# Kernel optimization log

Measured on AMD Instinct MI355X. Metric: run time of the kernel, lower is better.

## Reference

```python
import jax, jax.numpy as jnp
import numpy as np

B, C, CE, DK, DV, H, W = 2, 64, 96, 64, 64, 96, 96
EPS = 1e-6


def setup_inputs() -> dict:
    key = jax.random.key(0)
    ks = jax.random.split(key, 8)
    s = lambda fan_in: 1.0 / np.sqrt(fan_in)
    return {
        "x": jax.random.normal(ks[0], (B, C, H, W), jnp.float32),
        "x_enc": jax.random.normal(ks[1], (B, CE, H, W), jnp.float32),
        "Wq": jax.random.uniform(ks[2], (DK, CE), jnp.float32, -s(CE), s(CE)),
        "bq": jax.random.uniform(ks[3], (DK,), jnp.float32, -s(CE), s(CE)),
        "Wk": jax.random.uniform(ks[4], (DK, CE), jnp.float32, -s(CE), s(CE)),
        "bk": jax.random.uniform(ks[5], (DK,), jnp.float32, -s(CE), s(CE)),
        "Wv": jax.random.uniform(ks[6], (DV, C), jnp.float32, -s(C), s(C)),
        "bv": jax.random.uniform(ks[7], (DV,), jnp.float32, -s(C), s(C)),
    }


def _l2norm(t):
    # F.normalize(dim=1): divide by channel-dim L2 norm, clamped at eps
    n = jnp.maximum(jnp.linalg.norm(t, axis=1, keepdims=True), EPS)
    return t / n


def reference(x, x_enc, Wq, bq, Wk, bk, Wv, bv):
    # 1x1 conv projections == pointwise channel GEMMs
    Q = jnp.einsum('oc,bchw->bohw', Wq, x_enc) + bq[None, :, None, None]
    K = jnp.einsum('oc,bchw->bohw', Wk, x_enc) + bk[None, :, None, None]
    V = jnp.einsum('oc,bchw->bohw', Wv, x) + bv[None, :, None, None]
    vshape = V.shape
    Q = _l2norm(Q.reshape(B, DK, H * W))  # [B, dk, L]
    K = _l2norm(K.reshape(B, DK, H * W))
    V = V.reshape(B, DV, H * W)           # [B, dv, L]
    # cosine-similarity attention over all spatial positions: A is [B, L, L]
    A = jax.nn.softmax(jnp.einsum('bqi,bqj->bij', Q, K), axis=-1)
    R = jnp.einsum('bij,bvj->bvi', A, V)   # [B, dv, L]
    return R.reshape(vshape)
```

## Files before the change

kernel.cpp:

```cpp
#include <hip/hip_runtime.h>

#define L_ 9216

typedef unsigned int uint;
typedef unsigned short ushort;
typedef __attribute__((ext_vector_type(8))) short short8;
typedef __attribute__((ext_vector_type(4))) float f32x4;
typedef __attribute__((ext_vector_type(16))) float f32x16;
typedef __attribute__((ext_vector_type(4))) unsigned uint4v;
typedef __attribute__((ext_vector_type(2))) unsigned uint2v;

#define MFMA32(a, b, c) __builtin_amdgcn_mfma_f32_32x32x16_bf16(a, b, c, 0, 0, 0)

#if __has_builtin(__builtin_amdgcn_exp2f)
#define EXP2(x) __builtin_amdgcn_exp2f(x)
#else
#define EXP2(x) exp2f(x)
#endif

#define GLOAD_LDS16(g, l)                                            \
  __builtin_amdgcn_global_load_lds(                                  \
      (const __attribute__((address_space(1))) unsigned int*)(g),    \
      (__attribute__((address_space(3))) unsigned int*)(l), 16, 0, 0)

union B8 {
  uint4v u;
  short8 s;
};

__device__ __forceinline__ ushort f2bf(float f) {
  uint u = __float_as_uint(f);
  return (ushort)((u + 0x7fffu + ((u >> 16) & 1u)) >> 16);
}

__device__ __forceinline__ f32x16 zero16() {
  f32x16 v;
#pragma unroll
  for (int i = 0; i < 16; i++) v[i] = 0.f;
  return v;
}

__global__ __launch_bounds__(256) void prep_kernel(
    const float* __restrict__ Wq, const float* __restrict__ Wk,
    const float* __restrict__ Wv, ushort* __restrict__ Wqb,
    ushort* __restrict__ Wkb, ushort* __restrict__ Wvb) {
  int i = blockIdx.x * 256 + threadIdx.x;
  if (i < 6144) {
    Wqb[i] = f2bf(Wq[i]);
    Wkb[i] = f2bf(Wk[i]);
  }
  if (i < 4096) Wvb[i] = f2bf(Wv[i]);
}

template <int CC, int TASK>
__device__ __forceinline__ void projm_body(
    const float* __restrict__ X,
    const ushort* __restrict__ Wb,
    const float* __restrict__ bias,
    ushort* __restrict__ dst) {
  constexpr int NKT = CC / 16;
  const int bx = blockIdx.x;
  const int b = bx / 288;
  const int p0 = (bx - b * 288) * 32;
  const int lane = threadIdx.x;
  const int ql = lane & 31;
  const int hs = lane >> 5;

  const float* Xb = X + (size_t)b * CC * L_ + p0 + ql;
  float xv[NKT * 8];
#pragma unroll
  for (int kt = 0; kt < NKT; kt++)
#pragma unroll
    for (int i = 0; i < 8; i++)
      xv[kt * 8 + i] = Xb[(size_t)(kt * 16 + hs * 8 + i) * L_];

  B8 bfr[NKT];
#pragma unroll
  for (int kt = 0; kt < NKT; kt++)
#pragma unroll
    for (int j = 0; j < 4; j++) {
      uint lo = f2bf(xv[kt * 8 + 2 * j]);
      uint hi = f2bf(xv[kt * 8 + 2 * j + 1]);
      bfr[kt].u[j] = lo | (hi << 16);
    }

  const ushort* Wr0 = Wb + (size_t)ql * CC + hs * 8;
  const ushort* Wr1 = Wb + (size_t)(32 + ql) * CC + hs * 8;

  f32x16 a0 = zero16(), a1 = zero16();
#pragma unroll
  for (int kt = 0; kt < NKT; kt++) {
    short8 w0 = *(const short8*)(Wr0 + kt * 16);
    short8 w1 = *(const short8*)(Wr1 + kt * 16);
    a0 = MFMA32(w0, bfr[kt].s, a0);
    a1 = MFMA32(w1, bfr[kt].s, a1);
  }

#pragma unroll
  for (int g = 0; g < 4; g++) {
    float4 b0 = *(const float4*)(bias + 8 * g + 4 * hs);
    float4 b1 = *(const float4*)(bias + 32 + 8 * g + 4 * hs);
    a0[4 * g + 0] += b0.x; a0[4 * g + 1] += b0.y;
    a0[4 * g + 2] += b0.z; a0[4 * g + 3] += b0.w;
    a1[4 * g + 0] += b1.x; a1[4 * g + 1] += b1.y;
    a1[4 * g + 2] += b1.z; a1[4 * g + 3] += b1.w;
  }

  if (TASK < 2) {
    float ss = 0.f;
#pragma unroll
    for (int r = 0; r < 16; r++) ss += a0[r] * a0[r] + a1[r] * a1[r];
    ss += __shfl_xor(ss, 32);
    float i0 = 1.0f / fmaxf(sqrtf(ss), 1e-6f);
    if (TASK == 0) i0 *= 1.44269504f;
    uint* d = (uint*)(dst + ((size_t)(b * L_ + p0 + ql)) * 64);
#pragma unroll
    for (int g = 0; g < 4; g++) {
      uint2v u0, u1;
      u0[0] = (uint)f2bf(a0[4 * g + 0] * i0) | ((uint)f2bf(a0[4 * g + 1] * i0) << 16);
      u0[1] = (uint)f2bf(a0[4 * g + 2] * i0) | ((uint)f2bf(a0[4 * g + 3] * i0) << 16);
      u1[0] = (uint)f2bf(a1[4 * g + 0] * i0) | ((uint)f2bf(a1[4 * g + 1] * i0) << 16);
      u1[1] = (uint)f2bf(a1[4 * g + 2] * i0) | ((uint)f2bf(a1[4 * g + 3] * i0) << 16);
      *(uint2v*)(d + 4 * g + 2 * hs) = u0;
      *(uint2v*)(d + 16 + 4 * g + 2 * hs) = u1;
    }
  } else {
#pragma unroll
    for (int r = 0; r < 16; r++) {
      int dv0 = (r & 3) + 8 * (r >> 2) + 4 * hs;
      dst[(size_t)(b * 64 + dv0) * L_ + p0 + ql] = f2bf(a0[r]);
      dst[(size_t)(b * 64 + 32 + dv0) * L_ + p0 + ql] = f2bf(a1[r]);
    }
  }
}

__global__ __launch_bounds__(64) void projm_kernel(
    const float* __restrict__ x, const float* __restrict__ x_enc,
    const ushort* __restrict__ Wqb, const float* __restrict__ bq,
    const ushort* __restrict__ Wkb, const float* __restrict__ bk,
    const ushort* __restrict__ Wvb, const float* __restrict__ bv,
    ushort* __restrict__ Qb, ushort* __restrict__ Kb,
    ushort* __restrict__ Vb) {
  const int task = blockIdx.y;
  if (task == 0)
    projm_body<96, 0>(x_enc, Wqb, bq, Qb);
  else if (task == 1)
    projm_body<96, 1>(x_enc, Wkb, bk, Kb);
  else
    projm_body<64, 2>(x, Wvb, bv, Vb);
}

__global__ __launch_bounds__(512, 4) void attn_kernel(
    const ushort* __restrict__ Qb, const ushort* __restrict__ Kb,
    const ushort* __restrict__ Vb, ushort* __restrict__ OP,
    float* __restrict__ LB, int tps) {
  __shared__ __align__(16) ushort K_l[3][64 * 64];
  __shared__ __align__(16) ushort V_l[3][64 * 64];

  const int nwg = gridDim.x;
  const int chunk = nwg >> 3;
  const int bid = blockIdx.x;
  const int logical = (bid & 7) * chunk + (bid >> 3);
  const int split = logical / 72;
  const int qidx = logical - split * 72;
  const int b = qidx / 36;
  const int q0 = (qidx - b * 36) * 256;

  const int t = threadIdx.x;
  const int lane = t & 63;
  const int w = t >> 6;
  const int ql = lane & 31;
  const int hs = lane >> 5;

  const ushort* Kg = Kb + (size_t)b * L_ * 64;
  const ushort* Vg = Vb + (size_t)b * 64 * L_;

  const int qrow = q0 + w * 32 + ql;
  const ushort* Qr = Qb + ((size_t)(b * L_ + qrow)) * 64 + hs * 8;
  short8 qf[4];
  qf[0] = *(const short8*)(Qr);
  qf[1] = *(const short8*)(Qr + 16);
  qf[2] = *(const short8*)(Qr + 32);
  qf[3] = *(const short8*)(Qr + 48);

  B8 onesu;
  onesu.u[0] = 0x3F803F80u;
  onesu.u[1] = 0x3F803F80u;
  onesu.u[2] = 0x3F803F80u;
  onesu.u[3] = 0x3F803F80u;

  f32x16 o[2];
  o[0] = zero16();
  o[1] = zero16();
  f32x16 od = zero16();

  const int rr = t >> 3, pl = t & 7;
  const int psrc = (pl ^ (rr & 7)) << 3;
  const int j0base = split * tps * 64;

#define STAGE(buf, j0)                                                       \
  {                                                                          \
    GLOAD_LDS16(Kg + (size_t)(j0)*64 + rr * 64 + psrc, &K_l[buf][w * 512]);  \
    GLOAD_LDS16(Vg + (size_t)rr * L_ + (j0) + psrc, &V_l[buf][w * 512]);     \
  }

  STAGE(0, j0base);
  STAGE(1, j0base + 64);

  int cur = 0;
  for (int tt = 0; tt < tps; tt++) {
    if (tt + 1 < tps) {
      asm volatile("s_waitcnt vmcnt(2)" ::: "memory");
    } else {
      asm volatile("s_waitcnt vmcnt(0)" ::: "memory");
    }
    __builtin_amdgcn_s_barrier();
    __builtin_amdgcn_sched_barrier(0);
    if (tt + 2 < tps) {
      int nb = cur + 2;
      if (nb >= 3) nb -= 3;
      STAGE(nb, j0base + (tt + 2) * 64);
    }
    const ushort* Kc = K_l[cur];
    const ushort* Vc = V_l[cur];

    B8 pf[4];
#pragma unroll
    for (int st = 0; st < 2; st++) {
      const int krow = st * 32 + ql;
      const int ksw = (krow & 7) << 3;
      f32x16 sa = zero16();
      __builtin_amdgcn_s_setprio(1);
#pragma unroll
      for (int m = 0; m < 4; m++) {
        short8 kf = *(const short8*)&Kc[(krow * 64 + m * 16 + hs * 8) ^ ksw];
        sa = MFMA32(kf, qf[m], sa);
      }
      __builtin_amdgcn_s_setprio(0);
      uint Wp[8];
#pragma unroll
      for (int c = 0; c < 4; c++)
#pragma unroll
        for (int rp = 0; rp < 2; rp++) {
          int i0 = 4 * c + 2 * rp;
          float p0 = EXP2(sa[i0]);
          float p1 = EXP2(sa[i0 + 1]);
          Wp[2 * c + rp] = __builtin_amdgcn_perm(
              __float_as_uint(p1), __float_as_uint(p0), 0x07060302u);
        }
#pragma unroll
      for (int u = 0; u < 2; u++) {
        auto ra = __builtin_amdgcn_permlane32_swap(Wp[4 * u + 0], Wp[4 * u + 2],
                                                   false, false);
        auto rb = __builtin_amdgcn_permlane32_swap(Wp[4 * u + 1], Wp[4 * u + 3],
                                                   false, false);
        uint4v fw;
        fw[0] = ra[0];
        fw[1] = rb[0];
        fw[2] = ra[1];
        fw[3] = rb[1];
        pf[st * 2 + u].u = fw;
      }
    }

    __builtin_amdgcn_s_setprio(1);
#pragma unroll
    for (int s = 0; s < 4; s++) od = MFMA32(onesu.s, pf[s].s, od);

#pragma unroll
    for (int dt = 0; dt < 2; dt++) {
      const int vrow = dt * 32 + ql;
      const int vsw = (vrow & 7) << 3;
#pragma unroll
      for (int s = 0; s < 4; s++) {
        short8 vf = *(const short8*)&Vc[(vrow * 64 + s * 16 + hs * 8) ^ vsw];
        o[dt] = MFMA32(vf, pf[s].s, o[dt]);
      }
    }
    __builtin_amdgcn_s_setprio(0);

    cur = (cur + 1 == 3) ? 0 : cur + 1;
  }

  if (hs == 0) LB[(size_t)split * 2 * L_ + (size_t)b * L_ + qrow] = od[0];

  ushort* Ob = OP + (size_t)split * 2 * 64 * L_;
#pragma unroll
  for (int dt = 0; dt < 2; dt++)
#pragma unroll
    for (int r = 0; r < 16; r++) {
      int dv = dt * 32 + (r & 3) + 8 * (r >> 2) + 4 * hs;
      Ob[(size_t)(b * 64 + dv) * L_ + qrow] = f2bf(o[dt][r]);
    }
}

template <int NS>
__global__ __launch_bounds__(256) void combine_kernel(
    const ushort* __restrict__ OP, const float* __restrict__ LB,
    float* __restrict__ out) {
  const size_t e = ((size_t)blockIdx.x * 256 + threadIdx.x) * 8;
  const int bdv = (int)(e / L_);
  const int b = bdv >> 6;
  const int q = (int)(e % L_);
  float os[8], ls[8];
#pragma unroll
  for (int i = 0; i < 8; i++) { os[i] = 0.f; ls[i] = 0.f; }
#pragma unroll
  for (int s = 0; s < NS; s++) {
    uint4v pv = *(const uint4v*)(OP + (size_t)s * 2 * 64 * L_ + e);
    const float* lp = LB + (size_t)s * 2 * L_ + (size_t)b * L_ + q;
    f32x4 l0 = *(const f32x4*)(lp);
    f32x4 l1 = *(const f32x4*)(lp + 4);
#pragma unroll
    for (int i = 0; i < 4; i++) {
      os[2 * i] += __uint_as_float(pv[i] << 16);
      os[2 * i + 1] += __uint_as_float(pv[i] & 0xFFFF0000u);
      ls[i] += l0[i];
      ls[4 + i] += l1[i];
    }
  }
  float r[8];
#pragma unroll
  for (int i = 0; i < 8; i++) r[i] = os[i] / ls[i];
  *(f32x4*)(out + e) = *(const f32x4*)&r[0];
  *(f32x4*)(out + e + 4) = *(const f32x4*)&r[4];
}

extern "C" void kernel_launch(void* const* d_in, const int* in_sizes, int n_in,
                              void* d_out, int out_size, void* d_ws, size_t ws_size,
                              hipStream_t stream) {
  const float* x = (const float*)d_in[0];
  const float* x_enc = (const float*)d_in[1];
  const float* Wq = (const float*)d_in[2];
  const float* bq = (const float*)d_in[3];
  const float* Wk = (const float*)d_in[4];
  const float* bk = (const float*)d_in[5];
  const float* Wv = (const float*)d_in[6];
  const float* bv = (const float*)d_in[7];
  float* out = (float*)d_out;

  ushort* Qb = (ushort*)d_ws;
  ushort* Kb = Qb + (size_t)2 * L_ * 64;
  ushort* Vb = Kb + (size_t)2 * L_ * 64;
  ushort* Wqb = Vb + (size_t)2 * L_ * 64;
  ushort* Wkb = Wqb + 6144;
  ushort* Wvb = Wkb + 6144;
  const size_t qkv_bytes = (size_t)3 * 2 * L_ * 64 * 2 + 2 * (6144 + 6144 + 4096);
  const size_t per_split = (size_t)2 * 64 * L_ * 2 + (size_t)2 * L_ * 4;

  int SPLIT = 16;
  while (SPLIT > 1 && qkv_bytes + (size_t)SPLIT * per_split > ws_size) SPLIT >>= 1;

  ushort* OP = (ushort*)((char*)d_ws + qkv_bytes);
  float* LB = (float*)(OP + (size_t)SPLIT * 2 * 64 * L_);

  prep_kernel<<<24, 256, 0, stream>>>(Wq, Wk, Wv, Wqb, Wkb, Wvb);
  projm_kernel<<<dim3(576, 3), 64, 0, stream>>>(x, x_enc, Wqb, bq, Wkb, bk,
                                                Wvb, bv, Qb, Kb, Vb);
  attn_kernel<<<72 * SPLIT, 512, 0, stream>>>(Qb, Kb, Vb, OP, LB, 144 / SPLIT);
  const int cgrid = (2 * 64 * L_ / 8) / 256;
  if (SPLIT == 16)
    combine_kernel<16><<<cgrid, 256, 0, stream>>>(OP, LB, out);
  else if (SPLIT == 8)
    combine_kernel<8><<<cgrid, 256, 0, stream>>>(OP, LB, out);
  else if (SPLIT == 4)
    combine_kernel<4><<<cgrid, 256, 0, stream>>>(OP, LB, out);
  else if (SPLIT == 2)
    combine_kernel<2><<<cgrid, 256, 0, stream>>>(OP, LB, out);
  else
    combine_kernel<1><<<cgrid, 256, 0, stream>>>(OP, LB, out);
}
```

Baseline: 84.83 us.

## Give each attention wave two query tiles, halve block size, double-buffer K/V

Each wave now handles 64 query rows as two 32-row tiles and reuses every K and V fragment it reads from LDS for both tiles, which halves LDS reads per MFMA. The block shrinks to 256 threads, staging moves from a triple buffer to a double buffer with a plain __syncthreads, and each thread issues twice as many loads per stage. The row-sum is now accumulated in scalar registers and reduced with a lane shuffle, replacing the MFMA against a ones matrix. Register pressure roughly doubles and occupancy may fall, and the shallower pipeline may expose more load latency.

Result: slower. 89.57 us (+5.6%).

```diff
diff --git a/kernel.cpp b/kernel.cpp
--- a/kernel.cpp
+++ b/kernel.cpp
@@ -150,12 +150,12 @@
     projm_body<64, 2>(x, Wvb, bv, Vb);
 }
 
-__global__ __launch_bounds__(512, 4) void attn_kernel(
+__global__ __launch_bounds__(256) void attn_kernel(
     const ushort* __restrict__ Qb, const ushort* __restrict__ Kb,
     const ushort* __restrict__ Vb, ushort* __restrict__ OP,
     float* __restrict__ LB, int tps) {
-  __shared__ __align__(16) ushort K_l[3][64 * 64];
-  __shared__ __align__(16) ushort V_l[3][64 * 64];
+  __shared__ __align__(16) ushort K_l[2][4096];
+  __shared__ __align__(16) ushort V_l[2][4096];
 
   const int nwg = gridDim.x;
   const int chunk = nwg >> 3;
@@ -175,98 +175,92 @@
   const ushort* Kg = Kb + (size_t)b * L_ * 64;
   const ushort* Vg = Vb + (size_t)b * 64 * L_;
 
-  const int qrow = q0 + w * 32 + ql;
-  const ushort* Qr = Qb + ((size_t)(b * L_ + qrow)) * 64 + hs * 8;
-  short8 qf[4];
-  qf[0] = *(const short8*)(Qr);
-  qf[1] = *(const short8*)(Qr + 16);
-  qf[2] = *(const short8*)(Qr + 32);
-  qf[3] = *(const short8*)(Qr + 48);
-
-  B8 onesu;
-  onesu.u[0] = 0x3F803F80u;
-  onesu.u[1] = 0x3F803F80u;
-  onesu.u[2] = 0x3F803F80u;
-  onesu.u[3] = 0x3F803F80u;
-
-  f32x16 o[2];
-  o[0] = zero16();
-  o[1] = zero16();
-  f32x16 od = zero16();
+  const int qrowA = q0 + w * 64 + ql;
+  const int qrowB = qrowA + 32;
+  const ushort* QrA = Qb + ((size_t)(b * L_ + qrowA)) * 64 + hs * 8;
+  const ushort* QrB = Qb + ((size_t)(b * L_ + qrowB)) * 64 + hs * 8;
+  short8 qfA[4], qfB[4];
+#pragma unroll
+  for (int m = 0; m < 4; m++) {
+    qfA[m] = *(const short8*)(QrA + m * 16);
+    qfB[m] = *(const short8*)(QrB + m * 16);
+  }
+
+  f32x16 oA[2], oB[2];
+  oA[0] = zero16(); oA[1] = zero16();
+  oB[0] = zero16(); oB[1] = zero16();
+  float psA = 0.f, psB = 0.f;
 
   const int rr = t >> 3, pl = t & 7;
   const int psrc = (pl ^ (rr & 7)) << 3;
   const int j0base = split * tps * 64;
 
-#define STAGE(buf, j0)                                                       \
-  {                                                                          \
-    GLOAD_LDS16(Kg + (size_t)(j0)*64 + rr * 64 + psrc, &K_l[buf][w * 512]);  \
-    GLOAD_LDS16(Vg + (size_t)rr * L_ + (j0) + psrc, &V_l[buf][w * 512]);     \
+#define STAGE(buf, j0)                                                      \
+  {                                                                         \
+    GLOAD_LDS16(Kg + (size_t)(j0)*64 + rr * 64 + psrc, &K_l[buf][w * 512]); \
+    GLOAD_LDS16(Kg + (size_t)(j0)*64 + (rr + 32) * 64 + psrc,               \
+                &K_l[buf][2048 + w * 512]);                                 \
+    GLOAD_LDS16(Vg + (size_t)rr * L_ + (j0) + psrc, &V_l[buf][w * 512]);    \
+    GLOAD_LDS16(Vg + (size_t)(rr + 32) * L_ + (j0) + psrc,                  \
+                &V_l[buf][2048 + w * 512]);                                 \
+  }
+
+#define SMPACK(sa, ps, pf, st)                                              \
+  {                                                                         \
+    uint Wp[8];                                                             \
+    _Pragma("unroll") for (int c = 0; c < 4; c++) _Pragma("unroll")         \
+        for (int rp = 0; rp < 2; rp++) {                                    \
+      int i0 = 4 * c + 2 * rp;                                              \
+      float p0 = EXP2(sa[i0]);                                              \
+      float p1 = EXP2(sa[i0 + 1]);                                          \
+      ps += p0 + p1;                                                        \
+      Wp[2 * c + rp] = __builtin_amdgcn_perm(__float_as_uint(p1),           \
+                                             __float_as_uint(p0),           \
+                                             0x07060302u);                  \
+    }                                                                       \
+    _Pragma("unroll") for (int u = 0; u < 2; u++) {                         \
+      auto ra = __builtin_amdgcn_permlane32_swap(Wp[4 * u + 0],             \
+                                                 Wp[4 * u + 2], false,      \
+                                                 false);                    \
+      auto rb = __builtin_amdgcn_permlane32_swap(Wp[4 * u + 1],             \
+                                                 Wp[4 * u + 3], false,      \
+                                                 false);                    \
+      uint4v fw;                                                            \
+      fw[0] = ra[0];                                                        \
+      fw[1] = rb[0];                                                        \
+      fw[2] = ra[1];                                                        \
+      fw[3] = rb[1];                                                        \
+      pf[(st)*2 + u].u = fw;                                                \
+    }                                                                       \
   }
 
   STAGE(0, j0base);
-  STAGE(1, j0base + 64);
-
-  int cur = 0;
+
   for (int tt = 0; tt < tps; tt++) {
-    if (tt + 1 < tps) {
-      asm volatile("s_waitcnt vmcnt(2)" ::: "memory");
-    } else {
-      asm volatile("s_waitcnt vmcnt(0)" ::: "memory");
-    }
-    __builtin_amdgcn_s_barrier();
-    __builtin_amdgcn_sched_barrier(0);
-    if (tt + 2 < tps) {
-      int nb = cur + 2;
-      if (nb >= 3) nb -= 3;
-      STAGE(nb, j0base + (tt + 2) * 64);
-    }
-    const ushort* Kc = K_l[cur];
-    const ushort* Vc = V_l[cur];
-
-    B8 pf[4];
+    __syncthreads();
+    if (tt + 1 < tps) STAGE((tt + 1) & 1, j0base + (tt + 1) * 64);
+    const ushort* Kc = K_l[tt & 1];
+    const ushort* Vc = V_l[tt & 1];
+
+    B8 pfA[4], pfB[4];
 #pragma unroll
     for (int st = 0; st < 2; st++) {
       const int krow = st * 32 + ql;
       const int ksw = (krow & 7) << 3;
-      f32x16 sa = zero16();
+      f32x16 saA = zero16(), saB = zero16();
       __builtin_amdgcn_s_setprio(1);
 #pragma unroll
       for (int m = 0; m < 4; m++) {
         short8 kf = *(const short8*)&Kc[(krow * 64 + m * 16 + hs * 8) ^ ksw];
-        sa = MFMA32(kf, qf[m], sa);
+        saA = MFMA32(kf, qfA[m], saA);
+        saB = MFMA32(kf, qfB[m], saB);
       }
       __builtin_amdgcn_s_setprio(0);
-      uint Wp[8];
-#pragma unroll
-      for (int c = 0; c < 4; c++)
-#pragma unroll
-        for (int rp = 0; rp < 2; rp++) {
-          int i0 = 4 * c + 2 * rp;
-          float p0 = EXP2(sa[i0]);
-          float p1 = EXP2(sa[i0 + 1]);
-          Wp[2 * c + rp] = __builtin_amdgcn_perm(
-              __float_as_uint(p1), __float_as_uint(p0), 0x07060302u);
-        }
-#pragma unroll
-      for (int u = 0; u < 2; u++) {
-        auto ra = __builtin_amdgcn_permlane32_swap(Wp[4 * u + 0], Wp[4 * u + 2],
-                                                   false, false);
-        auto rb = __builtin_amdgcn_permlane32_swap(Wp[4 * u + 1], Wp[4 * u + 3],
-                                                   false, false);
-        uint4v fw;
-        fw[0] = ra[0];
-        fw[1] = rb[0];
-        fw[2] = ra[1];
-        fw[3] = rb[1];
-        pf[st * 2 + u].u = fw;
-      }
+      SMPACK(saA, psA, pfA, st);
+      SMPACK(saB, psB, pfB, st);
     }
 
     __builtin_amdgcn_s_setprio(1);
-#pragma unroll
-    for (int s = 0; s < 4; s++) od = MFMA32(onesu.s, pf[s].s, od);
-
 #pragma unroll
     for (int dt = 0; dt < 2; dt++) {
       const int vrow = dt * 32 + ql;
@@ -274,15 +268,20 @@
 #pragma unroll
       for (int s = 0; s < 4; s++) {
         short8 vf = *(const short8*)&Vc[(vrow * 64 + s * 16 + hs * 8) ^ vsw];
-        o[dt] = MFMA32(vf, pf[s].s, o[dt]);
+        oA[dt] = MFMA32(vf, pfA[s].s, oA[dt]);
+        oB[dt] = MFMA32(vf, pfB[s].s, oB[dt]);
       }
     }
     __builtin_amdgcn_s_setprio(0);
-
-    cur = (cur + 1 == 3) ? 0 : cur + 1;
-  }
-
-  if (hs == 0) LB[(size_t)split * 2 * L_ + (size_t)b * L_ + qrow] = od[0];
+  }
+
+  float pstA = psA + __shfl_xor(psA, 32);
+  float pstB = psB + __shfl_xor(psB, 32);
+  float* LBs = LB + (size_t)split * 2 * L_ + (size_t)b * L_;
+  if (hs == 0) {
+    LBs[qrowA] = pstA;
+    LBs[qrowB] = pstB;
+  }
 
   ushort* Ob = OP + (size_t)split * 2 * 64 * L_;
 #pragma unroll
@@ -290,7 +289,8 @@
 #pragma unroll
     for (int r = 0; r < 16; r++) {
       int dv = dt * 32 + (r & 3) + 8 * (r >> 2) + 4 * hs;
-      Ob[(size_t)(b * 64 + dv) * L_ + qrow] = f2bf(o[dt][r]);
+      Ob[(size_t)(b * 64 + dv) * L_ + qrowA] = f2bf(oA[dt][r]);
+      Ob[(size_t)(b * 64 + dv) * L_ + qrowB] = f2bf(oB[dt][r]);
     }
 }
 
@@ -357,7 +357,7 @@
   prep_kernel<<<24, 256, 0, stream>>>(Wq, Wk, Wv, Wqb, Wkb, Wvb);
   projm_kernel<<<dim3(576, 3), 64, 0, stream>>>(x, x_enc, Wqb, bq, Wkb, bk,
                                                 Wvb, bv, Qb, Kb, Vb);
-  attn_kernel<<<72 * SPLIT, 512, 0, stream>>>(Qb, Kb, Vb, OP, LB, 144 / SPLIT);
+  attn_kernel<<<72 * SPLIT, 256, 0, stream>>>(Qb, Kb, Vb, OP, LB, 144 / SPLIT);
   const int cgrid = (2 * 64 * L_ / 8) / 256;
   if (SPLIT == 16)
     combine_kernel<16><<<cgrid, 256, 0, stream>>>(OP, LB, out);
```
